# Optimization experiments

Measured on AMD Instinct MI355X. Metric: run time of the kernel, lower is better.

## Reference

```python
import jax, jax.numpy as jnp
import numpy as np

N_HARMONICS = 128
N_STEPS = 1024
N_SAMPLES = 262144


def setup_inputs() -> dict:
    key = jax.random.key(0)
    k1, k2 = jax.random.split(key)
    scores = jax.random.uniform(k1, (N_SAMPLES,), dtype=jnp.float32)  # scores assumed in [0,1]
    targets = jax.random.bernoulli(k2, 0.5, (N_SAMPLES,))
    return {"scores": scores, "targets": targets}


def _chain_fourier(s_basis, c_basis, mask, two_pi_k):
    """compute_fourier + normalize_by_samples + integrate (termwise) for one class.

    s_basis/c_basis: (K, N) precomputed sin/cos(2*pi*k*s); mask: (N,) float 0/1.
    Masked sum == ragged nonzero+gather in the original, same math.
    """
    eps = jnp.finfo(jnp.float32).eps
    n = jnp.sum(mask)
    safe_n = jnp.maximum(n, eps)
    # _norm_or_pass: zero coefficients if the class is empty, else divide by count
    sin_c = jnp.where(n < eps, 0.0, (s_basis @ mask) / safe_n)  # (K,)
    cos_c = jnp.where(n < eps, 0.0, (c_basis @ mask) / safe_n)
    # termwise integration of sum_k [sin_c sin(wx) + cos_c cos(wx)], w = 2*pi*k:
    # int sin(wx) dx = -cos(wx)/w ; int cos(wx) dx = sin(wx)/w
    int_sin = cos_c / two_pi_k
    int_cos = -sin_c / two_pi_k
    return int_sin, int_cos


def _normalized_cdf(thrs, sin_c, cos_c, two_pi_k):
    # evaluate_fourier on n_steps thresholds, then normalize_cdf: [1, 1-0.5*(cdf+0.5), 0]
    ang = thrs[:, None] * two_pi_k[None, :]  # (S, K)
    cdf = jnp.sin(ang) @ sin_c + jnp.cos(ang) @ cos_c  # (S,)
    one = jnp.ones((1,), dtype=cdf.dtype)
    zero = jnp.zeros((1,), dtype=cdf.dtype)
    return jnp.concatenate([one, 1.0 - 0.5 * (cdf + 0.5), zero])


def reference(scores, targets):
    two_pi_k = 2.0 * jnp.pi * jnp.arange(1, N_HARMONICS + 1, dtype=jnp.float32)  # (K,)
    ang = two_pi_k[:, None] * scores[None, :]  # (K, N) dominant intermediate
    s_basis = jnp.sin(ang)
    c_basis = jnp.cos(ang)
    pos_mask = targets.astype(jnp.float32)
    neg_mask = 1.0 - pos_mask
    ps, pc = _chain_fourier(s_basis, c_basis, pos_mask, two_pi_k)
    ns, nc = _chain_fourier(s_basis, c_basis, neg_mask, two_pi_k)
    thrs = jnp.linspace(0.0, 1.0, N_STEPS, dtype=jnp.float32)
    pos_norm = _normalized_cdf(thrs, ps, pc, two_pi_k)  # (S+2,)
    neg_norm = _normalized_cdf(thrs, ns, nc, two_pi_k)
    # AUC via Riemann integration of one CDF against the other
    pos_auc = jnp.sum(pos_norm[:-1] * (-jnp.diff(neg_norm)))
    neg_auc = 1.0 + jnp.sum(neg_norm[:-1] * jnp.diff(pos_norm))
    # statistic == 'flatten': single column -> flatten scalar to shape (1,)
    return jnp.reshape(0.5 * (pos_auc + neg_auc), (1,))
```

## Files before the change

### kernel.cpp

```cpp
#include <hip/hip_runtime.h>
#include <hip/hip_bf16.h>


#define NK 128
#define NSTEPS 1024
#define K1_TPB 256
#define CHUNK 512
#define PSTRIDE 520
#define DET_BLOCKS 32
#define DET_TPB 256
#define K2_TPB 1024

__device__ __forceinline__ float wave_sum(float v) {
  #pragma unroll
  for (int off = 32; off > 0; off >>= 1) v += __shfl_down(v, off, 64);
  return v;
}

__device__ __forceinline__ float block_sum(float v, float* scratch) {
  int lane = threadIdx.x & 63, wid = threadIdx.x >> 6;
  v = wave_sum(v);
  if (lane == 0) scratch[wid] = v;
  __syncthreads();
  float r = 0.0f;
  if (threadIdx.x == 0) {
    int nw = blockDim.x >> 6;
    for (int w = 0; w < nw; ++w) r += scratch[w];
  }
  return r;
}

__global__ __launch_bounds__(DET_TPB) void k_detect(const unsigned char* __restrict__ t,
                                                    int nbytes,
                                                    unsigned* __restrict__ flags) {
  __shared__ unsigned s_or;
  if (threadIdx.x == 0) s_or = 0u;
  __syncthreads();
  unsigned local = 0u;
  int n16 = nbytes >> 4;
  const uint4* p = (const uint4*)t;
  for (int i = blockIdx.x * DET_TPB + threadIdx.x; i < n16; i += DET_BLOCKS * DET_TPB) {
    uint4 v = p[i];
    local |= v.x | v.y | v.z | v.w;
  }
  if (blockIdx.x == 0 && threadIdx.x < (nbytes & 15)) {
    int i = (n16 << 4) + threadIdx.x;
    local |= ((unsigned)t[i]) << ((i & 3) * 8);
  }
  if (local) atomicOr(&s_or, local);
  __syncthreads();
  if (threadIdx.x == 0) flags[blockIdx.x] = s_or;
}

__device__ __forceinline__ int decode_mode(const unsigned* __restrict__ flags) {
  unsigned o = 0u;
  #pragma unroll
  for (int i = 0; i < DET_BLOCKS; ++i) o |= flags[i];
  bool nz0 = (o & 0xFFu) != 0u;
  bool nz1 = (o & 0xFF00u) != 0u;
  bool nz23 = (o & 0xFFFF0000u) != 0u;
  if (!nz1 && !nz23) return 1;
  if (!nz0 && !nz1) return 2;
  return 0;
}

__global__ __launch_bounds__(K1_TPB) void k_partial(const float* __restrict__ scores,
                                                    const unsigned char* __restrict__ tgt,
                                                    int N,
                                                    const unsigned* __restrict__ flags,
                                                    float* __restrict__ partials) {
  __shared__ float2 s_d[CHUNK];
  __shared__ float s_comb[NK * 4];
  __shared__ float s_red[K1_TPB / 64];
  const int mode = decode_mode(flags);
  const int base = blockIdx.x * CHUNK;

  float lc = 0.0f;
  for (int i = threadIdx.x; i < CHUNK; i += K1_TPB) {
    int g = base + i;
    float s = 0.0f, m = 0.0f;
    if (g < N) {
      s = scores[g];
      if (mode == 0)      m = (float)tgt[g];
      else if (mode == 1) m = (float)((const int*)tgt)[g];
      else                m = ((const float*)tgt)[g];
    }
    s_d[i] = make_float2(s, m);
    lc += m;
  }
  __syncthreads();
  float cnt = block_sum(lc, s_red);

  const int k_idx = threadIdx.x & (NK - 1);
  const int half = threadIdx.x >> 7;
  const float kf = (float)(k_idx + 1);
  const int HC = CHUNK / 2;
  const int i0 = half * HC;

  float ps = 0.0f, pc = 0.0f, ts = 0.0f, tc = 0.0f;
  #pragma unroll 4
  for (int i = 0; i < HC; ++i) {
    float2 d = s_d[i0 + i];
    float x = kf * d.x;
    float f = __builtin_amdgcn_fractf(x);
    float sn = __builtin_amdgcn_sinf(f);
    float cs = __builtin_amdgcn_cosf(f);
    ts += sn;
    tc += cs;
    ps = fmaf(d.y, sn, ps);
    pc = fmaf(d.y, cs, pc);
  }
  int valid = min(max(N - base - i0, 0), HC);
  tc -= (float)(HC - valid);

  if (half == 1) {
    s_comb[k_idx * 4 + 0] = ps;
    s_comb[k_idx * 4 + 1] = pc;
    s_comb[k_idx * 4 + 2] = ts;
    s_comb[k_idx * 4 + 3] = tc;
  }
  __syncthreads();
  float* ob = partials + (size_t)blockIdx.x * PSTRIDE;
  if (half == 0) {
    float4 o;
    o.x = ps + s_comb[k_idx * 4 + 0];
    o.y = pc + s_comb[k_idx * 4 + 1];
    o.z = ts + s_comb[k_idx * 4 + 2];
    o.w = tc + s_comb[k_idx * 4 + 3];
    ((float4*)ob)[k_idx] = o;
  }
  if (threadIdx.x == 0) ob[NK * 4] = cnt;
}

__global__ __launch_bounds__(K2_TPB) void k_final(const float* __restrict__ partials,
                                                  int nblocks, int N,
                                                  float* __restrict__ out) {
  __shared__ float s_tmp[K2_TPB];
  __shared__ float s_sums[NK * 4];
  __shared__ float s_isp[NK], s_icp[NK], s_isn[NK], s_icn[NK];
  __shared__ float s_pn[NSTEPS + 2], s_nn[NSTEPS + 2];
  __shared__ float s_red[K2_TPB / 64];
  __shared__ float s_npos;
  const int tid = threadIdx.x;

  {
    int q = tid & 511;
    int hb = tid >> 9;
    int bph = (nblocks + 1) >> 1;
    int b0 = hb * bph;
    int b1 = min(nblocks, b0 + bph);
    float acc = 0.0f;
    #pragma unroll 8
    for (int b = b0; b < b1; ++b) acc += partials[(size_t)b * PSTRIDE + q];
    s_tmp[tid] = acc;
  }
  float cl = 0.0f;
  for (int b = tid; b < nblocks; b += K2_TPB) cl += partials[(size_t)b * PSTRIDE + NK * 4];
  __syncthreads();
  if (tid < NK * 4) s_sums[tid] = s_tmp[tid] + s_tmp[tid + 512];
  float np = block_sum(cl, s_red);
  if (tid == 0) s_npos = np;
  __syncthreads();

  if (tid < NK) {
    const float eps = 1.1920929e-07f;
    float npos = s_npos;
    float nneg = (float)N - npos;
    float sp = s_sums[tid * 4 + 0], cp = s_sums[tid * 4 + 1];
    float st = s_sums[tid * 4 + 2], ct = s_sums[tid * 4 + 3];
    float scp, ccp, scn, ccn;
    if (npos < eps) { scp = 0.0f; ccp = 0.0f; }
    else { float d = fmaxf(npos, eps); scp = sp / d; ccp = cp / d; }
    if (nneg < eps) { scn = 0.0f; ccn = 0.0f; }
    else { float d = fmaxf(nneg, eps); scn = (st - sp) / d; ccn = (ct - cp) / d; }
    float w = 6.2831853071795864769f * (float)(tid + 1);
    s_isp[tid] = ccp / w;  s_icp[tid] = -scp / w;
    s_isn[tid] = ccn / w;  s_icn[tid] = -scn / w;
  }
  __syncthreads();

  {
    float thr = (float)tid * (1.0f / 1023.0f);
    float cp_acc = 0.0f, cn_acc = 0.0f;
    #pragma unroll 4
    for (int k = 0; k < NK; ++k) {
      float x = (float)(k + 1) * thr;
      float f = __builtin_amdgcn_fractf(x);
      float sn = __builtin_amdgcn_sinf(f);
      float cs = __builtin_amdgcn_cosf(f);
      cp_acc += sn * s_isp[k] + cs * s_icp[k];
      cn_acc += sn * s_isn[k] + cs * s_icn[k];
    }
    s_pn[tid + 1] = 1.0f - 0.5f * (cp_acc + 0.5f);
    s_nn[tid + 1] = 1.0f - 0.5f * (cn_acc + 0.5f);
  }
  if (tid == 0) {
    s_pn[0] = 1.0f; s_nn[0] = 1.0f;
    s_pn[NSTEPS + 1] = 0.0f; s_nn[NSTEPS + 1] = 0.0f;
  }
  __syncthreads();

  float pa = 0.0f, na = 0.0f;
  for (int i = tid; i < NSTEPS + 1; i += K2_TPB) {
    float p0 = s_pn[i], p1 = s_pn[i + 1];
    float n0 = s_nn[i], n1 = s_nn[i + 1];
    pa = fmaf(p0, n0 - n1, pa);
    na = fmaf(n0, p1 - p0, na);
  }
  float paS = block_sum(pa, s_red);
  __syncthreads();
  float naS = block_sum(na, s_red);
  if (tid == 0) out[0] = 0.5f * (paS + (1.0f + naS));
}

extern "C" void kernel_launch(void* const* d_in, const int* in_sizes, int n_in,
                              void* d_out, int out_size, void* d_ws, size_t ws_size,
                              hipStream_t stream) {
  const float* scores = (const float*)d_in[0];
  const unsigned char* targets = (const unsigned char*)d_in[1];
  const int N = in_sizes[0];

  unsigned* flags = (unsigned*)d_ws;
  float* partials = (float*)((char*)d_ws + 1024);

  const int nblocks = (N + CHUNK - 1) / CHUNK;

  k_detect<<<DET_BLOCKS, DET_TPB, 0, stream>>>(targets, N, flags);
  k_partial<<<nblocks, K1_TPB, 0, stream>>>(scores, targets, N, flags, partials);
  k_final<<<1, K2_TPB, 0, stream>>>(partials, nblocks, N, (float*)d_out);
}
```

Measured before the change: 99.09 us.

## Replace per-block partial buffer with global atomic accumulation and single-block mode detect

Blocks of the main pass now atomically add their per-harmonic sums and counts into one small global accumulator instead of writing a strided partials array. The final kernel then just reads the accumulated values instead of reducing over all blocks. Target-type detection moves to a single 1024-thread block that computes the mode once and also zeroes the accumulator. This trades the final-kernel serial reduction for atomic contention on a few hundred addresses and a slower single-block detect pass, and makes float summation order nondeterministic.

```diff
diff --git a/kernel.cpp b/kernel.cpp
--- a/kernel.cpp
+++ b/kernel.cpp
@@ -6,9 +6,7 @@
 #define NSTEPS 1024
 #define K1_TPB 256
 #define CHUNK 512
-#define PSTRIDE 520
-#define DET_BLOCKS 32
-#define DET_TPB 256
+#define DET_TPB 1024
 #define K2_TPB 1024
 
 __device__ __forceinline__ float wave_sum(float v) {
@@ -32,47 +30,52 @@
 
 __global__ __launch_bounds__(DET_TPB) void k_detect(const unsigned char* __restrict__ t,
                                                     int nbytes,
-                                                    unsigned* __restrict__ flags) {
+                                                    unsigned* __restrict__ mode_out,
+                                                    float* __restrict__ acc) {
   __shared__ unsigned s_or;
-  if (threadIdx.x == 0) s_or = 0u;
+  const int tid = threadIdx.x;
+  if (tid == 0) s_or = 0u;
+  if (tid < NK * 4 + 4) acc[tid] = 0.0f;
   __syncthreads();
   unsigned local = 0u;
   int n16 = nbytes >> 4;
   const uint4* p = (const uint4*)t;
-  for (int i = blockIdx.x * DET_TPB + threadIdx.x; i < n16; i += DET_BLOCKS * DET_TPB) {
+  for (int i = tid; i < n16; i += DET_TPB) {
     uint4 v = p[i];
     local |= v.x | v.y | v.z | v.w;
   }
-  if (blockIdx.x == 0 && threadIdx.x < (nbytes & 15)) {
-    int i = (n16 << 4) + threadIdx.x;
+  if (tid < (nbytes & 15)) {
+    int i = (n16 << 4) + tid;
     local |= ((unsigned)t[i]) << ((i & 3) * 8);
   }
   if (local) atomicOr(&s_or, local);
   __syncthreads();
-  if (threadIdx.x == 0) flags[blockIdx.x] = s_or;
-}
-
-__device__ __forceinline__ int decode_mode(const unsigned* __restrict__ flags) {
-  unsigned o = 0u;
-  #pragma unroll
-  for (int i = 0; i < DET_BLOCKS; ++i) o |= flags[i];
-  bool nz0 = (o & 0xFFu) != 0u;
-  bool nz1 = (o & 0xFF00u) != 0u;
-  bool nz23 = (o & 0xFFFF0000u) != 0u;
-  if (!nz1 && !nz23) return 1;
-  if (!nz0 && !nz1) return 2;
-  return 0;
+  if (tid == 0) {
+    unsigned o = s_or;
+    bool nz0 = (o & 0xFFu) != 0u;
+    bool nz1 = (o & 0xFF00u) != 0u;
+    bool nz23 = (o & 0xFFFF0000u) != 0u;
+    unsigned mode = 0u;
+    if (o != 0u) {
+      if (!nz1 && !nz23) mode = 1u;
+      else if (!nz0 && !nz1) mode = 2u;
+    }
+    mode_out[0] = mode;
+  }
 }
 
 __global__ __launch_bounds__(K1_TPB) void k_partial(const float* __restrict__ scores,
                                                     const unsigned char* __restrict__ tgt,
                                                     int N,
-                                                    const unsigned* __restrict__ flags,
-                                                    float* __restrict__ partials) {
+                                                    const unsigned* __restrict__ mode_ptr,
+                                                    float* __restrict__ acc) {
   __shared__ float2 s_d[CHUNK];
   __shared__ float s_comb[NK * 4];
   __shared__ float s_red[K1_TPB / 64];
-  const int mode = decode_mode(flags);
+  __shared__ unsigned s_mode;
+  if (threadIdx.x == 0) s_mode = mode_ptr[0];
+  __syncthreads();
+  const int mode = (int)s_mode;
   const int base = blockIdx.x * CHUNK;
 
   float lc = 0.0f;
@@ -120,22 +123,18 @@
     s_comb[k_idx * 4 + 3] = tc;
   }
   __syncthreads();
-  float* ob = partials + (size_t)blockIdx.x * PSTRIDE;
   if (half == 0) {
-    float4 o;
-    o.x = ps + s_comb[k_idx * 4 + 0];
-    o.y = pc + s_comb[k_idx * 4 + 1];
-    o.z = ts + s_comb[k_idx * 4 + 2];
-    o.w = tc + s_comb[k_idx * 4 + 3];
-    ((float4*)ob)[k_idx] = o;
-  }
-  if (threadIdx.x == 0) ob[NK * 4] = cnt;
-}
-
-__global__ __launch_bounds__(K2_TPB) void k_final(const float* __restrict__ partials,
-                                                  int nblocks, int N,
+    atomicAdd(&acc[k_idx * 4 + 0], ps + s_comb[k_idx * 4 + 0]);
+    atomicAdd(&acc[k_idx * 4 + 1], pc + s_comb[k_idx * 4 + 1]);
+    atomicAdd(&acc[k_idx * 4 + 2], ts + s_comb[k_idx * 4 + 2]);
+    atomicAdd(&acc[k_idx * 4 + 3], tc + s_comb[k_idx * 4 + 3]);
+  }
+  if (threadIdx.x == 0) atomicAdd(&acc[NK * 4], cnt);
+}
+
+__global__ __launch_bounds__(K2_TPB) void k_final(const float* __restrict__ acc,
+                                                  int N,
                                                   float* __restrict__ out) {
-  __shared__ float s_tmp[K2_TPB];
   __shared__ float s_sums[NK * 4];
   __shared__ float s_isp[NK], s_icp[NK], s_isn[NK], s_icn[NK];
   __shared__ float s_pn[NSTEPS + 2], s_nn[NSTEPS + 2];
@@ -143,23 +142,8 @@
   __shared__ float s_npos;
   const int tid = threadIdx.x;
 
-  {
-    int q = tid & 511;
-    int hb = tid >> 9;
-    int bph = (nblocks + 1) >> 1;
-    int b0 = hb * bph;
-    int b1 = min(nblocks, b0 + bph);
-    float acc = 0.0f;
-    #pragma unroll 8
-    for (int b = b0; b < b1; ++b) acc += partials[(size_t)b * PSTRIDE + q];
-    s_tmp[tid] = acc;
-  }
-  float cl = 0.0f;
-  for (int b = tid; b < nblocks; b += K2_TPB) cl += partials[(size_t)b * PSTRIDE + NK * 4];
-  __syncthreads();
-  if (tid < NK * 4) s_sums[tid] = s_tmp[tid] + s_tmp[tid + 512];
-  float np = block_sum(cl, s_red);
-  if (tid == 0) s_npos = np;
+  if (tid < NK * 4) s_sums[tid] = acc[tid];
+  if (tid == 0) s_npos = acc[NK * 4];
   __syncthreads();
 
   if (tid < NK) {
@@ -220,12 +204,12 @@
   const unsigned char* targets = (const unsigned char*)d_in[1];
   const int N = in_sizes[0];
 
-  unsigned* flags = (unsigned*)d_ws;
-  float* partials = (float*)((char*)d_ws + 1024);
+  unsigned* mode_ptr = (unsigned*)d_ws;
+  float* acc = (float*)((char*)d_ws + 64);
 
   const int nblocks = (N + CHUNK - 1) / CHUNK;
 
-  k_detect<<<DET_BLOCKS, DET_TPB, 0, stream>>>(targets, N, flags);
-  k_partial<<<nblocks, K1_TPB, 0, stream>>>(scores, targets, N, flags, partials);
-  k_final<<<1, K2_TPB, 0, stream>>>(partials, nblocks, N, (float*)d_out);
-}
+  k_detect<<<1, DET_TPB, 0, stream>>>(targets, N, mode_ptr, acc);
+  k_partial<<<nblocks, K1_TPB, 0, stream>>>(scores, targets, N, mode_ptr, acc);
+  k_final<<<1, K2_TPB, 0, stream>>>(acc, N, (float*)d_out);
+}
```

Result: slower. 135.6 us (+36.9%).
